# Optimization experiments

Hardware: AMD Instinct MI355X
Metric: run time of the kernel (lower is better)

The kernel has to match this reference:

```python
import jax, jax.numpy as jnp
import numpy as np

NUM_HEADS = 16
E8_DIM = 8
NEG_INF = -1000000000.0


def _e8_roots():
    roots = []
    for i in range(8):
        for j in range(i + 1, 8):
            for si in (1.0, -1.0):
                for sj in (1.0, -1.0):
                    v = np.zeros(8)
                    v[i] = si
                    v[j] = sj
                    roots.append(v)
    for mask in range(256):
        if bin(mask).count('1') % 2 == 0:
            roots.append(np.array([0.5 if ((mask >> i) & 1) == 0 else -0.5 for i in range(8)]))
    return jnp.asarray(np.stack(roots), dtype=jnp.float32)  # [240, 8]

E8_ROOTS = _e8_roots()
E8_SQNORM = jnp.sum(E8_ROOTS ** 2, axis=-1)  # [240]


def nearest_e8(x):
    shp = x.shape
    xf = x.reshape(-1, E8_DIM)
    scores = -2.0 * (xf @ E8_ROOTS.T) + E8_SQNORM[None, :]  # [N, 240]
    idx = jnp.argmin(scores, axis=-1)
    return E8_ROOTS[idx].reshape(shp)


def setup_inputs() -> dict:
    key = jax.random.key(0)
    ks = jax.random.split(key, 8)
    B, T, D = 2, 2048, 1024
    hd = D // NUM_HEADS  # 64
    x = jax.random.normal(ks[0], (B, T, D), dtype=jnp.float32)
    s = 1.0 / np.sqrt(D)
    Wq = jax.random.normal(ks[1], (D, D), dtype=jnp.float32) * s
    Wk = jax.random.normal(ks[2], (D, D), dtype=jnp.float32) * s
    Wv = jax.random.normal(ks[3], (D, D), dtype=jnp.float32) * s
    Wout = jax.random.normal(ks[4], (D, D), dtype=jnp.float32) * s
    W_to_e8 = jax.random.normal(ks[5], (hd, E8_DIM), dtype=jnp.float32) * (1.0 / np.sqrt(hd))
    W_from_e8 = jax.random.normal(ks[6], (E8_DIM, hd), dtype=jnp.float32) * (1.0 / np.sqrt(E8_DIM))
    return {"x": x, "Wq": Wq, "Wk": Wk, "Wv": Wv, "W_to_e8": W_to_e8,
            "W_from_e8": W_from_e8, "Wout": Wout}


def reference(x, Wq, Wk, Wv, W_to_e8, W_from_e8, Wout):
    B, T, D = x.shape
    H = NUM_HEADS
    hd = D // H
    # QKV projections, split into heads: [B, H, T, hd]
    q = (x @ Wq).reshape(B, T, H, hd).transpose(0, 2, 1, 3)
    k = (x @ Wk).reshape(B, T, H, hd).transpose(0, 2, 1, 3)
    v = (x @ Wv).reshape(B, T, H, hd).transpose(0, 2, 1, 3)
    # E8 quantization of queries (head_dim 64 != 8 -> project to/from E8 space)
    q_e8 = q @ W_to_e8            # [B, H, T, 8]
    q_e8 = nearest_e8(q_e8)       # snap to nearest of 240 roots
    q = q_e8 @ W_from_e8          # [B, H, T, hd]
    scale = 1.0 / np.sqrt(hd)     # e8_attention_temperature = 1.0
    attn = jnp.einsum('bhqd,bhkd->bhqk', q, k) * scale
    mask = jnp.triu(jnp.ones((T, T), dtype=bool), k=1)
    attn = jnp.where(mask, NEG_INF, attn)
    attn = jax.nn.softmax(attn, axis=-1)
    out = jnp.einsum('bhqk,bhkd->bhqd', attn, v)
    out = out.transpose(0, 2, 1, 3).reshape(B, T, D)
    return out @ Wout
```

## Files before the change

### kernel.cpp

```cpp
#include <hip/hip_runtime.h>

typedef unsigned short u16;
typedef unsigned char  u8;
typedef unsigned int   u32;
typedef __attribute__((ext_vector_type(8))) short short8;
typedef __attribute__((ext_vector_type(4))) float f32x4;

__device__ __forceinline__ float bf2f(u16 u){
  union { u32 i; float f; } v; v.i = ((u32)u) << 16; return v.f;
}
__device__ __forceinline__ u16 f2bf(float f){
  union { float f; u32 i; } v; v.f = f;
  u32 x = v.i;
  x += 0x7fffu + ((x >> 16) & 1u);
  return (u16)(x >> 16);
}
__device__ __forceinline__ float loadin(const void* p, size_t i, int f){
  return f ? ((const float*)p)[i] : bf2f(((const u16*)p)[i]);
}
__device__ __forceinline__ void load8bf(const void* p, size_t i, int f, u16* dst){
  if (f){
    float4 a = *(const float4*)((const float*)p + i);
    float4 b = *(const float4*)((const float*)p + i + 4);
    dst[0]=f2bf(a.x); dst[1]=f2bf(a.y); dst[2]=f2bf(a.z); dst[3]=f2bf(a.w);
    dst[4]=f2bf(b.x); dst[5]=f2bf(b.y); dst[6]=f2bf(b.z); dst[7]=f2bf(b.w);
  } else {
    *(uint4*)dst = *(const uint4*)((const u16*)p + i);
  }
}

__global__ __launch_bounds__(256) void k_sniff(
    const u16* __restrict__ x, const void* __restrict__ e8a,
    const void* __restrict__ e8b, u32* __restrict__ flg)
{
  __shared__ int cnt[256];
  __shared__ float red[256];
  __shared__ int fsh;
  const int tid = threadIdx.x;
  int c = 0;
  const uint4* xv = (const uint4*)x;
  #pragma unroll 4
  for (int i = tid; i < 8192; i += 256){
    uint4 v = xv[i];
    c += (((v.x >>  7) & 0xFFu) == 0xFFu);
    c += (((v.x >> 23) & 0xFFu) == 0xFFu);
    c += (((v.y >>  7) & 0xFFu) == 0xFFu);
    c += (((v.y >> 23) & 0xFFu) == 0xFFu);
    c += (((v.z >>  7) & 0xFFu) == 0xFFu);
    c += (((v.z >> 23) & 0xFFu) == 0xFFu);
    c += (((v.w >>  7) & 0xFFu) == 0xFFu);
    c += (((v.w >> 23) & 0xFFu) == 0xFFu);
  }
  cnt[tid] = c;
  __syncthreads();
  for (int s = 128; s > 0; s >>= 1){
    if (tid < s) cnt[tid] += cnt[tid + s];
    __syncthreads();
  }
  if (tid == 0){
    int f = (cnt[0] >= 8) ? 1 : 0;
    flg[0] = (u32)f; fsh = f;
  }
  __syncthreads();
  const int f = fsh;
  float va = loadin(e8a, tid, f), vb = loadin(e8a, tid + 256, f);
  red[tid] = va * va + vb * vb;
  __syncthreads();
  for (int s = 128; s > 0; s >>= 1){
    if (tid < s) red[tid] += red[tid + s];
    __syncthreads();
  }
  if (tid == 0) flg[1] = (red[0] < 30.0f) ? 0u : 1u;
}

__device__ __forceinline__ void gen_root(int tid, float* v){
  #pragma unroll
  for (int q = 0; q < 8; q++) v[q] = 0.f;
  if (tid < 112){
    int pi = tid >> 2;
    int i = 0, p = pi;
    while (p >= 7 - i){ p -= 7 - i; i++; }
    int j = i + 1 + p;
    v[i] = (tid & 2) ? -1.f : 1.f;
    v[j] = (tid & 1) ? -1.f : 1.f;
  } else {
    int k = tid - 112;
    int mask = 2 * k + (__popc(k) & 1);
    #pragma unroll
    for (int q = 0; q < 8; q++) v[q] = ((mask >> q) & 1) ? -0.5f : 0.5f;
  }
}

__global__ __launch_bounds__(256) void k_prep_qrec(
    const void* __restrict__ e8a, const void* __restrict__ e8b,
    const u32* __restrict__ flg, float* __restrict__ Qrec)
{
  __shared__ float roots[240 * 8];
  __shared__ double wf[512];
  const int f = (int)flg[0], tid = threadIdx.x;
  const void* Wfrom = (flg[1] == 0u) ? e8b : e8a;
  if (tid < 240){
    float v[8];
    gen_root(tid, v);
    #pragma unroll
    for (int q = 0; q < 8; q++) roots[tid * 8 + q] = v[q];
  }
  wf[tid] = (double)loadin(Wfrom, tid, f);
  wf[tid + 256] = (double)loadin(Wfrom, tid + 256, f);
  __syncthreads();
  for (int e = tid; e < 240 * 64; e += 256){
    int r = e >> 6, d = e & 63;
    double acc = 0.0;
    #pragma unroll
    for (int j = 0; j < 8; j++)
      acc = fma((double)roots[r * 8 + j], wf[j * 64 + d], acc);
    Qrec[e] = (float)acc;
  }
}

__global__ __launch_bounds__(256) void k_prep_wqe(
    const void* __restrict__ Wq, const void* __restrict__ e8a,
    const void* __restrict__ e8b, const u32* __restrict__ flg,
    float* __restrict__ Wqe)
{
  __shared__ double wt[512];
  const int f = (int)flg[0], tid = threadIdx.x;
  const void* Wto = (flg[1] == 0u) ? e8a : e8b;
  wt[tid] = (double)loadin(Wto, tid, f);
  wt[tid + 256] = (double)loadin(Wto, tid + 256, f);
  __syncthreads();
  int g = blockIdx.x * 256 + tid;
  int j = g & 7, h = (g >> 3) & 15, d = g >> 7;
  double s = 0.0;
  for (int d2 = 0; d2 < 64; d2++)
    s = fma((double)loadin(Wq, (size_t)d * 1024 + h * 64 + d2, f), wt[d2 * 8 + j], s);
  Wqe[(size_t)d * 128 + h * 8 + j] = (float)s;
}

__global__ __launch_bounds__(256) void k_qe8(
    const void* __restrict__ x, const u32* __restrict__ flg,
    const float* __restrict__ Wqe, u8* __restrict__ Qidx)
{
  __shared__ float xs[4 * 1088];
  __shared__ float roots[240 * 8];
  double* xw   = (double*)xs;
  double* totb = (double*)xs + 48 * 33;
  const int f = (int)flg[0], tid = threadIdx.x;
  if (tid < 240){
    float v[8];
    gen_root(tid, v);
    #pragma unroll
    for (int q = 0; q < 8; q++) roots[tid * 8 + q] = v[q];
  }
  const int m0 = blockIdx.x * 4;
  {
    const int e = tid * 16;
    const int rr = e >> 10, cc = e & 1023;
    const size_t g = (size_t)(m0 + rr) * 1024 + cc;
    float* dstp = xs + rr * 1088 + cc + ((cc >> 6) << 2);
    if (f){
      #pragma unroll
      for (int u = 0; u < 4; u++)
        *(float4*)(dstp + u * 4) = *(const float4*)((const float*)x + g + u * 4);
    } else {
      #pragma unroll
      for (int u = 0; u < 2; u++){
        union { uint4 u4; u16 us[8]; } t;
        t.u4 = *(const uint4*)((const u16*)x + g + u * 8);
        #pragma unroll
        for (int jj = 0; jj < 8; jj++) dstp[u * 8 + jj] = bf2f(t.us[jj]);
      }
    }
  }
  __syncthreads();
  const int h = tid & 15, ks = tid >> 4;
  float acc[4][8];
  #pragma unroll
  for (int r = 0; r < 4; r++)
    #pragma unroll
    for (int j = 0; j < 8; j++) acc[r][j] = 0.f;
  {
    const float* xrow = xs + ks * 68;
    const float* wq = Wqe + (size_t)(ks * 64) * 128 + h * 8;
    for (int d8 = 0; d8 < 64; d8 += 8){
      float xv[4][8];
      #pragma unroll
      for (int r = 0; r < 4; r++){
        *(float4*)(xv[r])     = *(const float4*)(xrow + r * 1088 + d8);
        *(float4*)(xv[r] + 4) = *(const float4*)(xrow + r * 1088 + d8 + 4);
      }
      #pragma unroll
      for (int u = 0; u < 8; u++){
        float wv[8];
        *(float4*)(wv)     = *(const float4*)(wq + (size_t)(d8 + u) * 128);
        *(float4*)(wv + 4) = *(const float4*)(wq + (size_t)(d8 + u) * 128 + 4);
        #pragma unroll
        for (int r = 0; r < 4; r++){
          float xd = xv[r][u];
          #pragma unroll
          for (int j = 0; j < 8; j++)
            acc[r][j] = fmaf(xd, wv[j], acc[r][j]);
        }
      }
    }
  }
  double accd[4][8];
  #pragma unroll
  for (int r = 0; r < 4; r++)
    #pragma unroll
    for (int j = 0; j < 8; j++){
      double v = (double)acc[r][j];
      v += __shfl_xor(v, 16);
      v += __shfl_xor(v, 32);
      accd[r][j] = v;
    }
  __syncthreads();
  const int lane = tid & 63, wid = tid >> 6;
  if (wid >= 1 && lane < 16){
    double* dst = xw + ((wid - 1) * 16 + lane) * 33;
    #pragma unroll
    for (int r = 0; r < 4; r++)
      #pragma unroll
      for (int j = 0; j < 8; j++) dst[r * 8 + j] = accd[r][j];
  }
  __syncthreads();
  if (wid == 0 && lane < 16){
    #pragma unroll
    for (int r = 0; r < 4; r++)
      #pragma unroll
      for (int j = 0; j < 8; j++){
        double t = (accd[r][j]                   + xw[(lane) * 33 + r * 8 + j])
                 + (xw[(16 + lane) * 33 + r * 8 + j] + xw[(32 + lane) * 33 + r * 8 + j]);
        totb[(r * 16 + lane) * 9 + j] = t;
      }
  }
  __syncthreads();
  const int unit = tid >> 2, s = tid & 3;
  double t8[8];
  #pragma unroll
  for (int j = 0; j < 8; j++) t8[j] = totb[unit * 9 + j];
  double best = 1.0e300; int bi = 0;
  const int rt0 = s * 60;
  for (int rt = rt0; rt < rt0 + 60; rt++){
    const float* rp = roots + rt * 8;
    double d = 0.0;
    #pragma unroll
    for (int j = 0; j < 8; j++) d = fma(t8[j], (double)rp[j], d);
    double sc = -2.0 * d + 2.0;
    if (sc < best){ best = sc; bi = rt; }
  }
  {
    double ob = __shfl_xor(best, 1); int oi = __shfl_xor(bi, 1);
    if (ob < best || (ob == best && oi < bi)){ best = ob; bi = oi; }
    ob = __shfl_xor(best, 2); oi = __shfl_xor(bi, 2);
    if (ob < best || (ob == best && oi < bi)){ best = ob; bi = oi; }
  }
  if (s == 0){
    const int row_local = unit >> 4, hh = unit & 15;
    const int m = m0 + row_local, b = m >> 11, t = m & 2047;
    Qidx[(size_t)(b * 16 + hh) * 2048 + t] = (u8)bi;
  }
}

__global__ __launch_bounds__(256) void k_cvt_wT(
    const void* __restrict__ W0, const void* __restrict__ W1,
    const void* __restrict__ W2, const u32* __restrict__ flg,
    u16* __restrict__ WT)
{
  __shared__ u16 Ts[64 * 72];
  const int f = (int)flg[0];
  const void* src = (blockIdx.y == 0) ? W0 : (blockIdx.y == 1) ? W1 : W2;
  u16* dst = WT + (size_t)blockIdx.y * (1024 * 1024);
  const int rt = blockIdx.x >> 4, ct = blockIdx.x & 15;
  const int tid = threadIdx.x;
  #pragma unroll
  for (int half = 0; half < 2; half++){
    int c = tid + half * 256;
    int r = c >> 3, cc = (c & 7) * 8;
    u16 t8[8];
    load8bf(src, (size_t)(rt * 64 + r) * 1024 + ct * 64 + cc, f, t8);
    *(uint4*)(Ts + r * 72 + cc) = *(uint4*)t8;
  }
  __syncthreads();
  #pragma unroll
  for (int half = 0; half < 2; half++){
    int c = tid + half * 256;
    int r = c >> 3, cc = (c & 7) * 8;
    union { uint4 u4; u16 us[8]; } t;
    #pragma unroll
    for (int jj = 0; jj < 8; jj++) t.us[jj] = Ts[(cc + jj) * 72 + r];
    *(uint4*)(dst + (size_t)(ct * 64 + r) * 1024 + rt * 64 + cc) = t.u4;
  }
}

__device__ __forceinline__ void gemm_core_bt(
    const void* __restrict__ A, int af, const u16* __restrict__ Bt,
    u16* As, u16* Bs, int bm, int bn, f32x4 (&acc)[4][4])
{
  const int tid = threadIdx.x;
  const int lane = tid & 63, w = tid >> 6;
  const int wm = w >> 1, wn = w & 1, quad = lane >> 4, l15 = lane & 15;
  #pragma unroll
  for (int mt = 0; mt < 4; mt++)
    #pragma unroll
    for (int nt = 0; nt < 4; nt++) acc[mt][nt] = (f32x4){0.f, 0.f, 0.f, 0.f};
  const int r0 = tid >> 2, c0 = (tid & 3) * 8;
  const u16* Br0 = Bt + (size_t)(bn * 128 + r0) * 1024 + c0;
  const u16* Br1 = Bt + (size_t)(bn * 128 + r0 + 64) * 1024 + c0;
  u16* wA0 = As + r0 * 40 + c0;
  u16* wA1 = As + (r0 + 64) * 40 + c0;
  u16* wB0 = Bs + r0 * 40 + c0;
  u16* wB1 = Bs + (r0 + 64) * 40 + c0;
  for (int k0 = 0; k0 < 1024; k0 += 32){
    u16 t8[8];
    load8bf(A, (size_t)(bm * 128 + r0) * 1024 + k0 + c0, af, t8);
    *(uint4*)wA0 = *(uint4*)t8;
    load8bf(A, (size_t)(bm * 128 + r0 + 64) * 1024 + k0 + c0, af, t8);
    *(uint4*)wA1 = *(uint4*)t8;
    *(uint4*)wB0 = *(const uint4*)(Br0 + k0);
    *(uint4*)wB1 = *(const uint4*)(Br1 + k0);
    __syncthreads();
    short8 afr[4];
    #pragma unroll
    for (int mt = 0; mt < 4; mt++)
      afr[mt] = *(const short8*)(As + (wm * 64 + mt * 16 + l15) * 40 + quad * 8);
    #pragma unroll
    for (int nt = 0; nt < 4; nt++){
      short8 bfr = *(const short8*)(Bs + (wn * 64 + nt * 16 + l15) * 40 + quad * 8);
      #pragma unroll
      for (int mt = 0; mt < 4; mt++)
        acc[mt][nt] = __builtin_amdgcn_mfma_f32_16x16x32_bf16(afr[mt], bfr, acc[mt][nt], 0, 0, 0);
    }
    __syncthreads();
  }
}

__global__ __launch_bounds__(256) void k_gemm_kv(
    const void* __restrict__ X, const u16* __restrict__ WkT,
    const u16* __restrict__ WvT, const u32* __restrict__ flg,
    u16* __restrict__ Kb, u16* __restrict__ Vb)
{
  __shared__ u16 lds[128 * 40 * 2];
  const int f = (int)flg[0];
  const u16* Bt = (blockIdx.z == 0) ? WkT : WvT;
  f32x4 acc[4][4];
  gemm_core_bt(X, f, Bt, lds, lds + 128 * 40, blockIdx.y, blockIdx.x, acc);
  const int tid = threadIdx.x, lane = tid & 63, w = tid >> 6;
  const int wm = w >> 1, wn = w & 1, quad = lane >> 4, l15 = lane & 15;
  u16* dst = (blockIdx.z == 0) ? Kb : Vb;
  #pragma unroll
  for (int mt = 0; mt < 4; mt++)
    #pragma unroll
    for (int nt = 0; nt < 4; nt++)
      #pragma unroll
      for (int rr = 0; rr < 4; rr++){
        int m = blockIdx.y * 128 + wm * 64 + mt * 16 + quad * 4 + rr;
        int n = blockIdx.x * 128 + wn * 64 + nt * 16 + l15;
        int b = m >> 11, t = m & 2047, h = n >> 6, d = n & 63;
        dst[((size_t)(b * 16 + h) * 2048 + t) * 64 + d] = f2bf(acc[mt][nt][rr]);
      }
}

__global__ __launch_bounds__(256) void k_gemm_out(
    const u16* __restrict__ A, const u16* __restrict__ WoutT,
    float* __restrict__ O)
{
  __shared__ u16 lds[128 * 40 * 2];
  f32x4 acc[4][4];
  gemm_core_bt(A, 0, WoutT, lds, lds + 128 * 40, blockIdx.y, blockIdx.x, acc);
  const int tid = threadIdx.x, lane = tid & 63, w = tid >> 6;
  const int wm = w >> 1, wn = w & 1, quad = lane >> 4, l15 = lane & 15;
  #pragma unroll
  for (int mt = 0; mt < 4; mt++)
    #pragma unroll
    for (int nt = 0; nt < 4; nt++)
      #pragma unroll
      for (int rr = 0; rr < 4; rr++){
        int m = blockIdx.y * 128 + wm * 64 + mt * 16 + quad * 4 + rr;
        int n = blockIdx.x * 128 + wn * 64 + nt * 16 + l15;
        O[(size_t)m * 1024 + n] = acc[mt][nt][rr];
      }
}

__global__ __launch_bounds__(256) void k_vt(
    const u16* __restrict__ Vb, u16* __restrict__ Vt)
{
  __shared__ u16 Ts[64 * 72];
  const int tt = blockIdx.x, bh = blockIdx.y;
  const int tid = threadIdx.x;
  #pragma unroll
  for (int half = 0; half < 2; half++){
    int e = tid + half * 256;
    int r = e >> 3, c = (e & 7) * 8;
    *(uint4*)(Ts + r * 72 + c) =
        *(const uint4*)(Vb + ((size_t)bh * 2048 + tt * 64 + r) * 64 + c);
  }
  __syncthreads();
  #pragma unroll
  for (int half = 0; half < 2; half++){
    int e = tid + half * 256;
    int d = e >> 3, t0 = (e & 7) * 8;
    union { uint4 u4; u16 us[8]; } t;
    #pragma unroll
    for (int jj = 0; jj < 8; jj++) t.us[jj] = Ts[(t0 + jj) * 72 + d];
    *(uint4*)(Vt + (size_t)bh * (64 * 2048) + (size_t)d * 2048 + tt * 64 + t0) = t.u4;
  }
}

__global__ __launch_bounds__(256) void k_flash(
    const u8* __restrict__ Qidx, const float* __restrict__ Qrec,
    const u16* __restrict__ Kb, const u16* __restrict__ Vt,
    u16* __restrict__ AO)
{
  __shared__ u16 lds[23040];
  u16* Ks0 = lds;
  u16* Ks1 = lds + 4608;
  u16* Vs0 = lds + 9216;
  u16* Vs1 = lds + 13824;
  u16* Ps  = lds + 18432;
  const int tid = threadIdx.x;
  const int lane = tid & 63, w = tid >> 6, quad = lane >> 4, l15 = lane & 15;
  const int bx = blockIdx.x, bh = blockIdx.y;
  const size_t baseK = (size_t)bh * (2048 * 64);
  const size_t baseV = (size_t)bh * (64 * 2048);
  const int sr = tid >> 3, sc = (tid & 7) * 8;
  const int b = bh >> 4, h = bh & 15;
  u16* Pw = Ps + w * (16 * 72);
  #pragma unroll
  for (int ph = 0; ph < 2; ph++){
    const int qt = ph ? (31 - bx) : bx;
    const int qrowA = qt * 64 + w * 16 + l15;
    const int qi = Qidx[bh * 2048 + qrowA];
    const float* qr = Qrec + qi * 64;
    u16 qtmp[8];
    float4 qa = *(const float4*)(qr + quad * 8);
    float4 qb = *(const float4*)(qr + quad * 8 + 4);
    qtmp[0]=f2bf(qa.x); qtmp[1]=f2bf(qa.y); qtmp[2]=f2bf(qa.z); qtmp[3]=f2bf(qa.w);
    qtmp[4]=f2bf(qb.x); qtmp[5]=f2bf(qb.y); qtmp[6]=f2bf(qb.z); qtmp[7]=f2bf(qb.w);
    short8 aq0 = *(short8*)qtmp;
    qa = *(const float4*)(qr + 32 + quad * 8);
    qb = *(const float4*)(qr + 32 + quad * 8 + 4);
    qtmp[0]=f2bf(qa.x); qtmp[1]=f2bf(qa.y); qtmp[2]=f2bf(qa.z); qtmp[3]=f2bf(qa.w);
    qtmp[4]=f2bf(qb.x); qtmp[5]=f2bf(qb.y); qtmp[6]=f2bf(qb.z); qtmp[7]=f2bf(qb.w);
    short8 aq1 = *(short8*)qtmp;
    f32x4 o[4];
    #pragma unroll
    for (int nt = 0; nt < 4; nt++) o[nt] = (f32x4){0.f, 0.f, 0.f, 0.f};
    float lpart[4] = {0.f, 0.f, 0.f, 0.f};
    const int qrow_q = qt * 64 + w * 16 + quad * 4;
    #pragma unroll
    for (int half = 0; half < 2; half++){
      int r = sr + half * 32;
      *(uint4*)(Ks0 + r * 72 + sc) =
          *(const uint4*)(Kb + baseK + (size_t)r * 64 + sc);
      *(uint4*)(Vs0 + r * 72 + sc) =
          *(const uint4*)(Vt + baseV + (size_t)r * 2048 + sc);
    }
    __syncthreads();
    for (int kt = 0; kt <= qt; kt++){
      const int kbase = kt * 64;
      const int cur = kt & 1;
      u16* Kc = cur ? Ks1 : Ks0;
      u16* Vc = cur ? Vs1 : Vs0;
      u16* Kn = cur ? Ks0 : Ks1;
      u16* Vn = cur ? Vs0 : Vs1;
      const bool pf = (kt < qt);
      uint4 kr0, kr1, vr0, vr1;
      if (pf){
        const int nb = kbase + 64;
        kr0 = *(const uint4*)(Kb + baseK + (size_t)(nb + sr) * 64 + sc);
        kr1 = *(const uint4*)(Kb + baseK + (size_t)(nb + sr + 32) * 64 + sc);
        vr0 = *(const uint4*)(Vt + baseV + (size_t)sr * 2048 + nb + sc);
        vr1 = *(const uint4*)(Vt + baseV + (size_t)(sr + 32) * 2048 + nb + sc);
      }
      f32x4 s[4];
      #pragma unroll
      for (int nt = 0; nt < 4; nt++){
        s[nt] = (f32x4){0.f, 0.f, 0.f, 0.f};
        short8 bk0 = *(const short8*)(Kc + (nt * 16 + l15) * 72 + quad * 8);
        short8 bk1 = *(const short8*)(Kc + (nt * 16 + l15) * 72 + 32 + quad * 8);
        s[nt] = __builtin_amdgcn_mfma_f32_16x16x32_bf16(aq0, bk0, s[nt], 0, 0, 0);
        s[nt] = __builtin_amdgcn_mfma_f32_16x16x32_bf16(aq1, bk1, s[nt], 0, 0, 0);
      }
      if (kt == qt){
        #pragma unroll
        for (int rr = 0; rr < 4; rr++)
          #pragma unroll
          for (int nt = 0; nt < 4; nt++){
            float p = (kbase + nt * 16 + l15 > qrow_q + rr)
                        ? 0.f : __expf(s[nt][rr] * 0.125f - 16.0f);
            lpart[rr] += p;
            Pw[(quad * 4 + rr) * 72 + nt * 16 + l15] = f2bf(p);
          }
      } else {
        #pragma unroll
        for (int rr = 0; rr < 4; rr++)
          #pragma unroll
          for (int nt = 0; nt < 4; nt++){
            float p = __expf(s[nt][rr] * 0.125f - 16.0f);
            lpart[rr] += p;
            Pw[(quad * 4 + rr) * 72 + nt * 16 + l15] = f2bf(p);
          }
      }
      #pragma unroll
      for (int ks = 0; ks < 2; ks++){
        short8 pa = *(const short8*)(Pw + l15 * 72 + ks * 32 + quad * 8);
        #pragma unroll
        for (int nt = 0; nt < 4; nt++){
          short8 vbf = *(const short8*)(Vc + (nt * 16 + l15) * 72 + ks * 32 + quad * 8);
          o[nt] = __builtin_amdgcn_mfma_f32_16x16x32_bf16(pa, vbf, o[nt], 0, 0, 0);
        }
      }
      if (pf){
        *(uint4*)(Kn + sr * 72 + sc) = kr0;
        *(uint4*)(Kn + (sr + 32) * 72 + sc) = kr1;
        *(uint4*)(Vn + sr * 72 + sc) = vr0;
        *(uint4*)(Vn + (sr + 32) * 72 + sc) = vr1;
      }
      __syncthreads();
    }
    float linv[4];
    #pragma unroll
    for (int rr = 0; rr < 4; rr++){
      float L = lpart[rr];
      L += __shfl_xor(L, 1); L += __shfl_xor(L, 2);
      L += __shfl_xor(L, 4); L += __shfl_xor(L, 8);
      linv[rr] = 1.0f / L;
    }
    #pragma unroll
    for (int rr = 0; rr < 4; rr++){
      int qrow = qrow_q + rr;
      #pragma unroll
      for (int nt = 0; nt < 4; nt++){
        float v = o[nt][rr] * linv[rr];
        AO[(size_t)(b * 2048 + qrow) * 1024 + h * 64 + nt * 16 + l15] = f2bf(v);
      }
    }
  }
}

extern "C" void kernel_launch(void* const* d_in, const int* in_sizes, int n_in,
                              void* d_out, int out_size, void* d_ws, size_t ws_size,
                              hipStream_t stream)
{
  int ix = -1, ibig[8], nbig = 0, i512[8], n512 = 0;
  for (int i = 0; i < n_in; i++){
    if (in_sizes[i] == 4194304) ix = i;
    else if (in_sizes[i] == 1048576){ if (nbig < 8) ibig[nbig++] = i; }
    else if (in_sizes[i] == 512){ if (n512 < 8) i512[n512++] = i; }
  }
  const void *x, *Wq, *Wk, *Wv, *Wout, *e8a, *e8b;
  if (ix >= 0 && nbig == 4 && n512 == 2){
    x = d_in[ix];
    e8a = d_in[i512[0]]; e8b = d_in[i512[1]];
    bool alpha = (i512[0] == 0 && i512[1] == 1 && ix == n_in - 1);
    if (alpha){
      Wk = d_in[ibig[0]]; Wout = d_in[ibig[1]];
      Wq = d_in[ibig[2]]; Wv   = d_in[ibig[3]];
    } else {
      Wq = d_in[ibig[0]]; Wk   = d_in[ibig[1]];
      Wv = d_in[ibig[2]]; Wout = d_in[ibig[3]];
    }
  } else {
    x = d_in[0]; Wq = d_in[1]; Wk = d_in[2]; Wv = d_in[3];
    e8a = d_in[4]; e8b = d_in[5]; Wout = d_in[6];
  }
  float* out = (float*)d_out;
  char* ws = (char*)d_ws;

  u32*   flg  = (u32*)  (ws);
  float* Qrec = (float*)(ws + 4096);
  u8*    Qidx = (u8*)   (ws + 69632);
  float* Wqe  = (float*)(ws + 147456);
  u16*   WT   = (u16*)  (ws + 1048576);
  u16*   Kb   = (u16*)  (ws + 7340032);
  u16*   Vb   = (u16*)  (ws + 15728640);
  u16*   Vt   = (u16*)  (ws + 24117248);
  u16*   AO   = (u16*)  (ws + 32505856);

  k_sniff<<<dim3(1), dim3(256), 0, stream>>>((const u16*)x, e8a, e8b, flg);
  k_prep_qrec<<<dim3(1), dim3(256), 0, stream>>>(e8a, e8b, flg, Qrec);
  k_prep_wqe<<<dim3(512), dim3(256), 0, stream>>>(Wq, e8a, e8b, flg, Wqe);
  k_qe8<<<dim3(1024), dim3(256), 0, stream>>>(x, flg, Wqe, Qidx);
  k_cvt_wT<<<dim3(256, 3), dim3(256), 0, stream>>>(Wk, Wv, Wout, flg, WT);
  k_gemm_kv<<<dim3(8, 32, 2), dim3(256), 0, stream>>>(
      x, WT, WT + 1048576, flg, Kb, Vb);
  k_vt<<<dim3(32, 32), dim3(256), 0, stream>>>(Vb, Vt);
  k_flash<<<dim3(16, 32), dim3(256), 0, stream>>>(Qidx, Qrec, Kb, Vt, AO);
  k_gemm_out<<<dim3(8, 32), dim3(256), 0, stream>>>(AO, WT + 2097152, out);
}
```

Baseline: 260.6 us.

## Double-buffer LDS tiles in shared GEMM core with register prefetch

```diff
diff --git a/kernel.cpp b/kernel.cpp
--- a/kernel.cpp
+++ b/kernel.cpp
@@ -295,8 +295,12 @@
 
 __device__ __forceinline__ void gemm_core_bt(
     const void* __restrict__ A, int af, const u16* __restrict__ Bt,
-    u16* As, u16* Bs, int bm, int bn, f32x4 (&acc)[4][4])
-{
+    u16* lds, int bm, int bn, f32x4 (&acc)[4][4])
+{
+  u16* As0 = lds;
+  u16* Bs0 = lds + 5120;
+  u16* As1 = lds + 10240;
+  u16* Bs1 = lds + 15360;
   const int tid = threadIdx.x;
   const int lane = tid & 63, w = tid >> 6;
   const int wm = w >> 1, wn = w & 1, quad = lane >> 4, l15 = lane & 15;
@@ -305,31 +309,54 @@
     #pragma unroll
     for (int nt = 0; nt < 4; nt++) acc[mt][nt] = (f32x4){0.f, 0.f, 0.f, 0.f};
   const int r0 = tid >> 2, c0 = (tid & 3) * 8;
+  const size_t aRow0 = (size_t)(bm * 128 + r0) * 1024 + c0;
+  const size_t aRow1 = (size_t)(bm * 128 + r0 + 64) * 1024 + c0;
   const u16* Br0 = Bt + (size_t)(bn * 128 + r0) * 1024 + c0;
   const u16* Br1 = Bt + (size_t)(bn * 128 + r0 + 64) * 1024 + c0;
-  u16* wA0 = As + r0 * 40 + c0;
-  u16* wA1 = As + (r0 + 64) * 40 + c0;
-  u16* wB0 = Bs + r0 * 40 + c0;
-  u16* wB1 = Bs + (r0 + 64) * 40 + c0;
+  const int wA0 = r0 * 40 + c0, wA1 = (r0 + 64) * 40 + c0;
+  {
+    u16 a0[8], a1[8];
+    load8bf(A, aRow0, af, a0);
+    load8bf(A, aRow1, af, a1);
+    uint4 b0 = *(const uint4*)(Br0);
+    uint4 b1 = *(const uint4*)(Br1);
+    *(uint4*)(As0 + wA0) = *(uint4*)a0;
+    *(uint4*)(As0 + wA1) = *(uint4*)a1;
+    *(uint4*)(Bs0 + wA0) = b0;
+    *(uint4*)(Bs0 + wA1) = b1;
+  }
+  __syncthreads();
   for (int k0 = 0; k0 < 1024; k0 += 32){
-    u16 t8[8];
-    load8bf(A, (size_t)(bm * 128 + r0) * 1024 + k0 + c0, af, t8);
-    *(uint4*)wA0 = *(uint4*)t8;
-    load8bf(A, (size_t)(bm * 128 + r0 + 64) * 1024 + k0 + c0, af, t8);
-    *(uint4*)wA1 = *(uint4*)t8;
-    *(uint4*)wB0 = *(const uint4*)(Br0 + k0);
-    *(uint4*)wB1 = *(const uint4*)(Br1 + k0);
-    __syncthreads();
+    const int cur = (k0 >> 5) & 1;
+    u16* Asc = cur ? As1 : As0;
+    u16* Bsc = cur ? Bs1 : Bs0;
+    u16* Asn = cur ? As0 : As1;
+    u16* Bsn = cur ? Bs0 : Bs1;
+    const bool pf = (k0 + 32 < 1024);
+    u16 na0[8], na1[8];
+    uint4 nb0, nb1;
+    if (pf){
+      load8bf(A, aRow0 + k0 + 32, af, na0);
+      load8bf(A, aRow1 + k0 + 32, af, na1);
+      nb0 = *(const uint4*)(Br0 + k0 + 32);
+      nb1 = *(const uint4*)(Br1 + k0 + 32);
+    }
     short8 afr[4];
     #pragma unroll
     for (int mt = 0; mt < 4; mt++)
-      afr[mt] = *(const short8*)(As + (wm * 64 + mt * 16 + l15) * 40 + quad * 8);
+      afr[mt] = *(const short8*)(Asc + (wm * 64 + mt * 16 + l15) * 40 + quad * 8);
     #pragma unroll
     for (int nt = 0; nt < 4; nt++){
-      short8 bfr = *(const short8*)(Bs + (wn * 64 + nt * 16 + l15) * 40 + quad * 8);
+      short8 bfr = *(const short8*)(Bsc + (wn * 64 + nt * 16 + l15) * 40 + quad * 8);
       #pragma unroll
       for (int mt = 0; mt < 4; mt++)
         acc[mt][nt] = __builtin_amdgcn_mfma_f32_16x16x32_bf16(afr[mt], bfr, acc[mt][nt], 0, 0, 0);
+    }
+    if (pf){
+      *(uint4*)(Asn + wA0) = *(uint4*)na0;
+      *(uint4*)(Asn + wA1) = *(uint4*)na1;
+      *(uint4*)(Bsn + wA0) = nb0;
+      *(uint4*)(Bsn + wA1) = nb1;
     }
     __syncthreads();
   }
@@ -340,11 +367,11 @@
     const u16* __restrict__ WvT, const u32* __restrict__ flg,
     u16* __restrict__ Kb, u16* __restrict__ Vb)
 {
-  __shared__ u16 lds[128 * 40 * 2];
+  __shared__ u16 lds[20480];
   const int f = (int)flg[0];
   const u16* Bt = (blockIdx.z == 0) ? WkT : WvT;
   f32x4 acc[4][4];
-  gemm_core_bt(X, f, Bt, lds, lds + 128 * 40, blockIdx.y, blockIdx.x, acc);
+  gemm_core_bt(X, f, Bt, lds, blockIdx.y, blockIdx.x, acc);
   const int tid = threadIdx.x, lane = tid & 63, w = tid >> 6;
   const int wm = w >> 1, wn = w & 1, quad = lane >> 4, l15 = lane & 15;
   u16* dst = (blockIdx.z == 0) ? Kb : Vb;
@@ -365,9 +392,9 @@
     const u16* __restrict__ A, const u16* __restrict__ WoutT,
     float* __restrict__ O)
 {
-  __shared__ u16 lds[128 * 40 * 2];
+  __shared__ u16 lds[20480];
   f32x4 acc[4][4];
-  gemm_core_bt(A, 0, WoutT, lds, lds + 128 * 40, blockIdx.y, blockIdx.x, acc);
+  gemm_core_bt(A, 0, WoutT, lds, blockIdx.y, blockIdx.x, acc);
   const int tid = threadIdx.x, lane = tid & 63, w = tid >> 6;
   const int wm = w >> 1, wn = w & 1, quad = lane >> 4, l15 = lane & 15;
   #pragma unroll
```

Measured after the change: 252.5 us. -3.1%, faster.
